# Optimization experiments

Hardware: AMD Instinct MI355X
Metric: run time of the kernel (lower is better)

Reference implementation:

```python
import jax, jax.numpy as jnp
import numpy as np


def setup_inputs() -> dict:
    key = jax.random.key(0)
    kx, kw = jax.random.split(key)
    x = jax.random.normal(kx, (65536, 4096), dtype=jnp.float32)  # [tokens, in_features]
    w = jax.random.normal(kw, (4096, 4096), dtype=jnp.float32)   # [out_features, in_features]
    return {"x": x, "w": w}


def reference(x, w):
    # Observer assumes fresh state: running min/max == current-batch min/max.
    # input_obs (ch_axis=1): per-column stats of x
    x_min = jnp.min(x, axis=0)  # [D]
    x_max = jnp.max(x, axis=0)  # [D]
    # weight_col_obs (ch_axis=1): per-column stats of w
    w_col_min = jnp.min(w, axis=0)  # [D]
    w_col_max = jnp.max(w, axis=0)  # [D]
    # weight_row_obs (ch_axis=0): per-row stats of w
    w_row_min = jnp.min(w, axis=1)  # [N]
    w_row_max = jnp.max(w, axis=1)  # [N]
    # Python loop of torch.where(w[i] == min_vals[i])[0][0] == first-occurrence
    # row argmin/argmax; vectorized here.
    min_weights_ind = jnp.argmin(w, axis=1).astype(jnp.int64)  # [N]
    max_weights_ind = jnp.argmax(w, axis=1).astype(jnp.int64)  # [N]
    return (x_min, x_max, w_col_min, w_col_max, w_row_min, w_row_max,
            min_weights_ind, max_weights_ind)
```

## Files before the change

### kernel.cpp

```cpp
#include <hip/hip_runtime.h>
#include <math.h>

#define COLS 4096
#define COLS4 (COLS / 4)

__global__ __launch_bounds__(256) void col_minmax_stage1(
    const float* __restrict__ src, int rows, int rows_per_chunk,
    float* __restrict__ ws_min, float* __restrict__ ws_max)
{
    int c4 = blockIdx.x * blockDim.x + threadIdx.x;
    if (c4 >= COLS4) return;
    int r0 = blockIdx.y * rows_per_chunk;
    int r1 = r0 + rows_per_chunk;
    if (r1 > rows) r1 = rows;

    float4 vmin = make_float4( INFINITY,  INFINITY,  INFINITY,  INFINITY);
    float4 vmax = make_float4(-INFINITY, -INFINITY, -INFINITY, -INFINITY);
    const float4* s4 = (const float4*)src;
    for (int r = r0; r < r1; ++r) {
        float4 v = s4[(size_t)r * COLS4 + c4];
        vmin.x = fminf(vmin.x, v.x); vmax.x = fmaxf(vmax.x, v.x);
        vmin.y = fminf(vmin.y, v.y); vmax.y = fmaxf(vmax.y, v.y);
        vmin.z = fminf(vmin.z, v.z); vmax.z = fmaxf(vmax.z, v.z);
        vmin.w = fminf(vmin.w, v.w); vmax.w = fmaxf(vmax.w, v.w);
    }
    size_t o = (size_t)blockIdx.y * COLS4 + c4;
    ((float4*)ws_min)[o] = vmin;
    ((float4*)ws_max)[o] = vmax;
}

__global__ __launch_bounds__(256) void col_minmax_stage2(
    const float* __restrict__ ws_min, const float* __restrict__ ws_max,
    int chunks, float* __restrict__ out_min, float* __restrict__ out_max)
{
    int c = blockIdx.x * blockDim.x + threadIdx.x;
    if (c >= COLS) return;
    float mn = INFINITY, mx = -INFINITY;
    for (int k = 0; k < chunks; ++k) {
        mn = fminf(mn, ws_min[(size_t)k * COLS + c]);
        mx = fmaxf(mx, ws_max[(size_t)k * COLS + c]);
    }
    out_min[c] = mn;
    out_max[c] = mx;
}

__global__ __launch_bounds__(256) void row_minmax_arg(
    const float* __restrict__ w,
    float* __restrict__ out_min, float* __restrict__ out_max,
    float* __restrict__ out_imin, float* __restrict__ out_imax)
{
    __shared__ float s_mn[256], s_mx[256];
    __shared__ int   s_in[256], s_ix[256];

    int row = blockIdx.x;
    const float4* w4 = (const float4*)(w + (size_t)row * COLS);

    float mn = INFINITY, mx = -INFINITY;
    int imn = 0, imx = 0;
    for (int i = threadIdx.x; i < COLS4; i += 256) {
        float4 v = w4[i];
        int b = i << 2;
        if (v.x < mn) { mn = v.x; imn = b;     }
        if (v.x > mx) { mx = v.x; imx = b;     }
        if (v.y < mn) { mn = v.y; imn = b + 1; }
        if (v.y > mx) { mx = v.y; imx = b + 1; }
        if (v.z < mn) { mn = v.z; imn = b + 2; }
        if (v.z > mx) { mx = v.z; imx = b + 2; }
        if (v.w < mn) { mn = v.w; imn = b + 3; }
        if (v.w > mx) { mx = v.w; imx = b + 3; }
    }

    int t = threadIdx.x;
    s_mn[t] = mn; s_in[t] = imn;
    s_mx[t] = mx; s_ix[t] = imx;
    __syncthreads();

    for (int s = 128; s > 0; s >>= 1) {
        if (t < s) {
            float ov = s_mn[t + s]; int oi = s_in[t + s];
            if (ov < s_mn[t] || (ov == s_mn[t] && oi < s_in[t])) { s_mn[t] = ov; s_in[t] = oi; }
            ov = s_mx[t + s]; oi = s_ix[t + s];
            if (ov > s_mx[t] || (ov == s_mx[t] && oi < s_ix[t])) { s_mx[t] = ov; s_ix[t] = oi; }
        }
        __syncthreads();
    }

    if (t == 0) {
        out_min[row]  = s_mn[0];
        out_max[row]  = s_mx[0];
        out_imin[row] = (float)s_in[0];
        out_imax[row] = (float)s_ix[0];
    }
}

extern "C" void kernel_launch(void* const* d_in, const int* in_sizes, int n_in,
                              void* d_out, int out_size, void* d_ws, size_t ws_size,
                              hipStream_t stream) {
    const float* x = (const float*)d_in[0];
    const float* w = (const float*)d_in[1];
    float* out = (float*)d_out;

    int rows_x = in_sizes[0] / COLS;
    int rows_w = in_sizes[1] / COLS;

    int chunks_x = 128, chunks_w = 32;
    size_t per = (size_t)COLS * 2 * sizeof(float);
    while ((size_t)(chunks_x + chunks_w) * per > ws_size && chunks_x > 4) {
        chunks_x >>= 1;
        if (chunks_w > 4) chunks_w >>= 1;
    }
    int rpc_x = (rows_x + chunks_x - 1) / chunks_x;
    int rpc_w = (rows_w + chunks_w - 1) / chunks_w;

    float* ws_min_x = (float*)d_ws;
    float* ws_max_x = ws_min_x + (size_t)chunks_x * COLS;
    float* ws_min_w = ws_max_x + (size_t)chunks_x * COLS;
    float* ws_max_w = ws_min_w + (size_t)chunks_w * COLS;

    float* x_min     = out + 0 * COLS;
    float* x_max     = out + 1 * COLS;
    float* w_col_min = out + 2 * COLS;
    float* w_col_max = out + 3 * COLS;
    float* w_row_min = out + 4 * COLS;
    float* w_row_max = out + 5 * COLS;
    float* w_imin    = out + 6 * COLS;
    float* w_imax    = out + 7 * COLS;

    dim3 blk(256);
    col_minmax_stage1<<<dim3(COLS4 / 256, chunks_x), blk, 0, stream>>>(
        x, rows_x, rpc_x, ws_min_x, ws_max_x);
    col_minmax_stage1<<<dim3(COLS4 / 256, chunks_w), blk, 0, stream>>>(
        w, rows_w, rpc_w, ws_min_w, ws_max_w);
    row_minmax_arg<<<dim3(rows_w), blk, 0, stream>>>(
        w, w_row_min, w_row_max, w_imin, w_imax);
    col_minmax_stage2<<<dim3(COLS / 256), blk, 0, stream>>>(
        ws_min_x, ws_max_x, chunks_x, x_min, x_max);
    col_minmax_stage2<<<dim3(COLS / 256), blk, 0, stream>>>(
        ws_min_w, ws_max_w, chunks_w, w_col_min, w_col_max);
}
```

Before: 1.548 ms.

## Restructure column min/max into full-row chunks with two-level partial reduction

Stage 1 now gives each block a full 4096-column row slab (four float4 per thread) over a smaller row range. The chunk count rises to 1024 for x and 256 for w, which exposes many more blocks and keeps more loads in flight per thread. The final reduction becomes a two-level tree of float4 reduce kernels instead of one serial loop over chunks per column. The workspace grows considerably, and the old ws_size guard is removed, so the code now assumes a large enough workspace. The row argmin/argmax loop is also fully unrolled.

Measured after the change: 1.418 ms. -8.4%, faster.

```diff
diff --git a/kernel.cpp b/kernel.cpp
--- a/kernel.cpp
+++ b/kernel.cpp
@@ -2,46 +2,69 @@
 #include <math.h>
 
 #define COLS 4096
-#define COLS4 (COLS / 4)
+#define COLS4 1024
 
 __global__ __launch_bounds__(256) void col_minmax_stage1(
     const float* __restrict__ src, int rows, int rows_per_chunk,
     float* __restrict__ ws_min, float* __restrict__ ws_max)
 {
-    int c4 = blockIdx.x * blockDim.x + threadIdx.x;
-    if (c4 >= COLS4) return;
-    int r0 = blockIdx.y * rows_per_chunk;
+    int chunk = blockIdx.x;
+    int r0 = chunk * rows_per_chunk;
     int r1 = r0 + rows_per_chunk;
     if (r1 > rows) r1 = rows;
 
-    float4 vmin = make_float4( INFINITY,  INFINITY,  INFINITY,  INFINITY);
-    float4 vmax = make_float4(-INFINITY, -INFINITY, -INFINITY, -INFINITY);
-    const float4* s4 = (const float4*)src;
-    for (int r = r0; r < r1; ++r) {
-        float4 v = s4[(size_t)r * COLS4 + c4];
-        vmin.x = fminf(vmin.x, v.x); vmax.x = fmaxf(vmax.x, v.x);
-        vmin.y = fminf(vmin.y, v.y); vmax.y = fmaxf(vmax.y, v.y);
-        vmin.z = fminf(vmin.z, v.z); vmax.z = fmaxf(vmax.z, v.z);
-        vmin.w = fminf(vmin.w, v.w); vmax.w = fmaxf(vmax.w, v.w);
+    float4 mn[4], mx[4];
+#pragma unroll
+    for (int j = 0; j < 4; ++j) {
+        mn[j] = make_float4( INFINITY,  INFINITY,  INFINITY,  INFINITY);
+        mx[j] = make_float4(-INFINITY, -INFINITY, -INFINITY, -INFINITY);
     }
-    size_t o = (size_t)blockIdx.y * COLS4 + c4;
-    ((float4*)ws_min)[o] = vmin;
-    ((float4*)ws_max)[o] = vmax;
+
+    const float4* p = (const float4*)src + (size_t)r0 * COLS4 + threadIdx.x;
+    for (int r = r0; r < r1; ++r, p += COLS4) {
+#pragma unroll
+        for (int j = 0; j < 4; ++j) {
+            float4 v = p[j * 256];
+            mn[j].x = fminf(mn[j].x, v.x); mx[j].x = fmaxf(mx[j].x, v.x);
+            mn[j].y = fminf(mn[j].y, v.y); mx[j].y = fmaxf(mx[j].y, v.y);
+            mn[j].z = fminf(mn[j].z, v.z); mx[j].z = fmaxf(mx[j].z, v.z);
+            mn[j].w = fminf(mn[j].w, v.w); mx[j].w = fmaxf(mx[j].w, v.w);
+        }
+    }
+
+    float4* omn = (float4*)ws_min + (size_t)chunk * COLS4 + threadIdx.x;
+    float4* omx = (float4*)ws_max + (size_t)chunk * COLS4 + threadIdx.x;
+#pragma unroll
+    for (int j = 0; j < 4; ++j) {
+        omn[j * 256] = mn[j];
+        omx[j * 256] = mx[j];
+    }
 }
 
-__global__ __launch_bounds__(256) void col_minmax_stage2(
-    const float* __restrict__ ws_min, const float* __restrict__ ws_max,
-    int chunks, float* __restrict__ out_min, float* __restrict__ out_max)
+__global__ __launch_bounds__(256) void col_minmax_reduce(
+    const float* __restrict__ in_min, const float* __restrict__ in_max,
+    int n_in, int cpg,
+    float* __restrict__ out_min, float* __restrict__ out_max)
 {
-    int c = blockIdx.x * blockDim.x + threadIdx.x;
-    if (c >= COLS) return;
-    float mn = INFINITY, mx = -INFINITY;
-    for (int k = 0; k < chunks; ++k) {
-        mn = fminf(mn, ws_min[(size_t)k * COLS + c]);
-        mx = fmaxf(mx, ws_max[(size_t)k * COLS + c]);
+    int c4 = blockIdx.x * 256 + threadIdx.x;
+    if (c4 >= COLS4) return;
+    int g = blockIdx.y;
+    int k0 = g * cpg;
+    int k1 = k0 + cpg;
+    if (k1 > n_in) k1 = n_in;
+
+    float4 mn = make_float4( INFINITY,  INFINITY,  INFINITY,  INFINITY);
+    float4 mx = make_float4(-INFINITY, -INFINITY, -INFINITY, -INFINITY);
+    for (int k = k0; k < k1; ++k) {
+        float4 a = ((const float4*)in_min)[(size_t)k * COLS4 + c4];
+        float4 b = ((const float4*)in_max)[(size_t)k * COLS4 + c4];
+        mn.x = fminf(mn.x, a.x); mx.x = fmaxf(mx.x, b.x);
+        mn.y = fminf(mn.y, a.y); mx.y = fmaxf(mx.y, b.y);
+        mn.z = fminf(mn.z, a.z); mx.z = fmaxf(mx.z, b.z);
+        mn.w = fminf(mn.w, a.w); mx.w = fmaxf(mx.w, b.w);
     }
-    out_min[c] = mn;
-    out_max[c] = mx;
+    ((float4*)out_min)[(size_t)g * COLS4 + c4] = mn;
+    ((float4*)out_max)[(size_t)g * COLS4 + c4] = mx;
 }
 
 __global__ __launch_bounds__(256) void row_minmax_arg(
@@ -57,7 +80,9 @@
 
     float mn = INFINITY, mx = -INFINITY;
     int imn = 0, imx = 0;
-    for (int i = threadIdx.x; i < COLS4; i += 256) {
+#pragma unroll
+    for (int u = 0; u < COLS4 / 256; ++u) {
+        int i = u * 256 + threadIdx.x;
         float4 v = w4[i];
         int b = i << 2;
         if (v.x < mn) { mn = v.x; imn = b;     }
@@ -103,19 +128,19 @@
     int rows_x = in_sizes[0] / COLS;
     int rows_w = in_sizes[1] / COLS;
 
-    int chunks_x = 128, chunks_w = 32;
-    size_t per = (size_t)COLS * 2 * sizeof(float);
-    while ((size_t)(chunks_x + chunks_w) * per > ws_size && chunks_x > 4) {
-        chunks_x >>= 1;
-        if (chunks_w > 4) chunks_w >>= 1;
-    }
+    const int chunks_x = 1024, g2_x = 32;
+    const int chunks_w = 256, g2_w = 8;
     int rpc_x = (rows_x + chunks_x - 1) / chunks_x;
     int rpc_w = (rows_w + chunks_w - 1) / chunks_w;
 
-    float* ws_min_x = (float*)d_ws;
-    float* ws_max_x = ws_min_x + (size_t)chunks_x * COLS;
-    float* ws_min_w = ws_max_x + (size_t)chunks_x * COLS;
-    float* ws_max_w = ws_min_w + (size_t)chunks_w * COLS;
+    float* ws_min_x  = (float*)d_ws;
+    float* ws_max_x  = ws_min_x  + (size_t)chunks_x * COLS;
+    float* ws2_min_x = ws_max_x  + (size_t)chunks_x * COLS;
+    float* ws2_max_x = ws2_min_x + (size_t)g2_x * COLS;
+    float* ws_min_w  = ws2_max_x + (size_t)g2_x * COLS;
+    float* ws_max_w  = ws_min_w  + (size_t)chunks_w * COLS;
+    float* ws2_min_w = ws_max_w  + (size_t)chunks_w * COLS;
+    float* ws2_max_w = ws2_min_w + (size_t)g2_w * COLS;
 
     float* x_min     = out + 0 * COLS;
     float* x_max     = out + 1 * COLS;
@@ -127,14 +152,21 @@
     float* w_imax    = out + 7 * COLS;
 
     dim3 blk(256);
-    col_minmax_stage1<<<dim3(COLS4 / 256, chunks_x), blk, 0, stream>>>(
+
+    col_minmax_stage1<<<dim3(chunks_x), blk, 0, stream>>>(
         x, rows_x, rpc_x, ws_min_x, ws_max_x);
-    col_minmax_stage1<<<dim3(COLS4 / 256, chunks_w), blk, 0, stream>>>(
+    col_minmax_stage1<<<dim3(chunks_w), blk, 0, stream>>>(
         w, rows_w, rpc_w, ws_min_w, ws_max_w);
     row_minmax_arg<<<dim3(rows_w), blk, 0, stream>>>(
         w, w_row_min, w_row_max, w_imin, w_imax);
-    col_minmax_stage2<<<dim3(COLS / 256), blk, 0, stream>>>(
-        ws_min_x, ws_max_x, chunks_x, x_min, x_max);
-    col_minmax_stage2<<<dim3(COLS / 256), blk, 0, stream>>>(
-        ws_min_w, ws_max_w, chunks_w, w_col_min, w_col_max);
+
+    col_minmax_reduce<<<dim3(COLS4 / 256, g2_x), blk, 0, stream>>>(
+        ws_min_x, ws_max_x, chunks_x, chunks_x / g2_x, ws2_min_x, ws2_max_x);
+    col_minmax_reduce<<<dim3(COLS4 / 256, 1), blk, 0, stream>>>(
+        ws2_min_x, ws2_max_x, g2_x, g2_x, x_min, x_max);
+
+    col_minmax_reduce<<<dim3(COLS4 / 256, g2_w), blk, 0, stream>>>(
+        ws_min_w, ws_max_w, chunks_w, chunks_w / g2_w, ws2_min_w, ws2_max_w);
+    col_minmax_reduce<<<dim3(COLS4 / 256, 1), blk, 0, stream>>>(
+        ws2_min_w, ws2_max_w, g2_w, g2_w, w_col_min, w_col_max);
 }
```
